# Optimization experiments

Measured on AMD Instinct MI355X. Metric: run time of the kernel, lower is better.

The kernel has to match this reference:

```python
import jax, jax.numpy as jnp
import numpy as np

B, N, D_IN, D_OUT = 4096, 200, 64, 64


def setup_inputs() -> dict:
    key = jax.random.key(0)
    k1, k2 = jax.random.split(key)
    x = jax.random.normal(k1, (B, N, D_IN), dtype=jnp.float32)
    # weight initialized like TF add_weight default (glorot-ish scale via normal here)
    weight = jax.random.normal(k2, (1, N, D_IN, D_OUT), dtype=jnp.float32) * (1.0 / np.sqrt(D_IN))
    bias = jnp.zeros((1, N, D_OUT), dtype=jnp.float32)
    return {"x": x, "weight": weight, "bias": bias}


def reference(x, weight, bias):
    # Original: (x[..., None] * weight).sum(-2) + bias
    # == per-token matmul: out[b,n,o] = sum_i x[b,n,i] * weight[0,n,i,o] + bias[0,n,o]
    out = jnp.einsum('bni,nio->bno', x, weight[0])
    return out + bias
```

## Files before the change

kernel.cpp:

```cpp
#include <hip/hip_runtime.h>


#define B_DIM 4096
#define N_DIM 200
#define D 64
#define ROWS_PER_BLOCK 256

typedef __attribute__((ext_vector_type(8))) _Float16 half8;
typedef __attribute__((ext_vector_type(4))) float f32x4;

__device__ __forceinline__ void split8(const float4 a, const float4 b,
                                       half8& h, half8& l) {
  const float f[8] = {a.x, a.y, a.z, a.w, b.x, b.y, b.z, b.w};
#pragma unroll
  for (int j = 0; j < 8; ++j) {
    const _Float16 hh = (_Float16)f[j];
    h[j] = hh;
    l[j] = (_Float16)(f[j] - (float)hh);
  }
}

__global__ __launch_bounds__(256)
void w_prep(const float* __restrict__ w,
            half8* __restrict__ wh, half8* __restrict__ wl) {
  const int n    = blockIdx.x;
  const int tid  = threadIdx.x;
  const int lane = tid & 63;
  const int g    = tid >> 6;
  const int c    = lane & 15;
  const int kg   = lane >> 4;
  const float* wn = w + (size_t)n * (D * D);
#pragma unroll
  for (int t = 0; t < 2; ++t) {
    const int combo = g * 2 + t;
    const int ks = combo >> 2;
    const int nf = combo & 3;
    half8 h, l;
#pragma unroll
    for (int j = 0; j < 8; ++j) {
      const int k = ks * 32 + kg * 8 + j;
      const float v = wn[k * D + nf * 16 + c];
      const _Float16 hh = (_Float16)v;
      h[j] = hh;
      l[j] = (_Float16)(v - (float)hh);
    }
    const size_t idx = ((size_t)(n * 2 + ks) * 4 + nf) * 64 + lane;
    wh[idx] = h;
    wl[idx] = l;
  }
}

template <bool PREPPED>
__global__ __launch_bounds__(256, 4)
void nlinear_main(const float* __restrict__ x,
                  const float* __restrict__ w,
                  const float* __restrict__ bias,
                  const half8* __restrict__ wh,
                  const half8* __restrict__ wl,
                  float* __restrict__ out) {
  const int n    = blockIdx.y;
  const int tid  = threadIdx.x;
  const int lane = tid & 63;
  const int wave = tid >> 6;
  const int c    = lane & 15;
  const int kg   = lane >> 4;

  half8 Wh[2][4], Wl[2][4];
  if (PREPPED) {
#pragma unroll
    for (int ks = 0; ks < 2; ++ks)
#pragma unroll
      for (int nf = 0; nf < 4; ++nf) {
        const size_t idx = ((size_t)(n * 2 + ks) * 4 + nf) * 64 + lane;
        Wh[ks][nf] = wh[idx];
        Wl[ks][nf] = wl[idx];
      }
  } else {
    const float* wn = w + (size_t)n * (D * D);
#pragma unroll
    for (int ks = 0; ks < 2; ++ks)
#pragma unroll
      for (int nf = 0; nf < 4; ++nf)
#pragma unroll
        for (int j = 0; j < 8; ++j) {
          const float v = wn[(ks * 32 + kg * 8 + j) * D + nf * 16 + c];
          const _Float16 hh = (_Float16)v;
          Wh[ks][nf][j] = hh;
          Wl[ks][nf][j] = (_Float16)(v - (float)hh);
        }
  }

  const float bv[4] = {bias[n * D + c],      bias[n * D + 16 + c],
                       bias[n * D + 32 + c], bias[n * D + 48 + c]};

  const size_t rstride = (size_t)N_DIM * D;
  const int row0 = blockIdx.x * ROWS_PER_BLOCK + wave * 64;
  const float* xb = x + (size_t)row0 * rstride + (size_t)n * D;
  float* ob = out + (size_t)row0 * rstride + (size_t)n * D;

  const float* xr0 = xb + (size_t)c * rstride + kg * 8;
  float4 A0 = *(const float4*)(xr0);
  float4 A1 = *(const float4*)(xr0 + 4);
  float4 A2 = *(const float4*)(xr0 + 32);
  float4 A3 = *(const float4*)(xr0 + 36);

#pragma unroll 1
  for (int mf = 0; mf < 4; ++mf) {
    const float4 v0 = A0, v1 = A1, v2 = A2, v3 = A3;
    if (mf < 3) {
      const float* xn = xb + (size_t)((mf + 1) * 16 + c) * rstride + kg * 8;
      A0 = *(const float4*)(xn);
      A1 = *(const float4*)(xn + 4);
      A2 = *(const float4*)(xn + 32);
      A3 = *(const float4*)(xn + 36);
    }

    half8 ah[2], al[2];
    split8(v0, v1, ah[0], al[0]);
    split8(v2, v3, ah[1], al[1]);

    f32x4 acc[4];
#pragma unroll
    for (int nf = 0; nf < 4; ++nf) {
      f32x4 t = {bv[nf], bv[nf], bv[nf], bv[nf]};
      acc[nf] = t;
    }

#pragma unroll
    for (int ks = 0; ks < 2; ++ks)
#pragma unroll
      for (int nf = 0; nf < 4; ++nf) {
        acc[nf] = __builtin_amdgcn_mfma_f32_16x16x32_f16(ah[ks], Wh[ks][nf], acc[nf], 0, 0, 0);
        acc[nf] = __builtin_amdgcn_mfma_f32_16x16x32_f16(ah[ks], Wl[ks][nf], acc[nf], 0, 0, 0);
        acc[nf] = __builtin_amdgcn_mfma_f32_16x16x32_f16(al[ks], Wh[ks][nf], acc[nf], 0, 0, 0);
      }

    float* orow = ob + (size_t)(mf * 16 + kg * 4) * rstride;
#pragma unroll
    for (int nf = 0; nf < 4; ++nf)
#pragma unroll
      for (int j = 0; j < 4; ++j)
        orow[(size_t)j * rstride + nf * 16 + c] = acc[nf][j];
  }
}

extern "C" void kernel_launch(void* const* d_in, const int* in_sizes, int n_in,
                              void* d_out, int out_size, void* d_ws, size_t ws_size,
                              hipStream_t stream) {
  const float* x    = (const float*)d_in[0];
  const float* w    = (const float*)d_in[1];
  const float* bias = (const float*)d_in[2];
  float*       out  = (float*)d_out;

  const size_t NFRAGS = (size_t)N_DIM * 2 * 4 * 64;
  const size_t NEED   = NFRAGS * 16 * 2;

  dim3 grid(B_DIM / ROWS_PER_BLOCK, N_DIM);
  if (d_ws && ws_size >= NEED) {
    half8* wh = (half8*)d_ws;
    half8* wl = wh + NFRAGS;
    w_prep<<<dim3(N_DIM), dim3(256), 0, stream>>>(w, wh, wl);
    nlinear_main<true><<<grid, dim3(256), 0, stream>>>(x, w, bias, wh, wl, out);
  } else {
    nlinear_main<false><<<grid, dim3(256), 0, stream>>>(x, w, bias, nullptr, nullptr, out);
  }
}
```

Before: 395.5 us.

## Transpose MFMA operands for vectorized float4 output stores and double-buffer x loads

Swaps the MFMA A/B operands so each lane's accumulator holds four consecutive output columns for one row. The epilogue can then write float4 stores instead of scalar strided stores, and bias is loaded as a float4. It also replaces the single-stage x prefetch with a two-deep register prefetch and fully unrolls the row loop. Occupancy is relaxed to 3 waves-per-EU in launch bounds to give room for the extra registers.

```diff
diff --git a/kernel.cpp b/kernel.cpp
--- a/kernel.cpp
+++ b/kernel.cpp
@@ -34,24 +34,24 @@
   for (int t = 0; t < 2; ++t) {
     const int combo = g * 2 + t;
     const int ks = combo >> 2;
-    const int nf = combo & 3;
+    const int of = combo & 3;
     half8 h, l;
 #pragma unroll
     for (int j = 0; j < 8; ++j) {
       const int k = ks * 32 + kg * 8 + j;
-      const float v = wn[k * D + nf * 16 + c];
+      const float v = wn[k * D + of * 16 + c];
       const _Float16 hh = (_Float16)v;
       h[j] = hh;
       l[j] = (_Float16)(v - (float)hh);
     }
-    const size_t idx = ((size_t)(n * 2 + ks) * 4 + nf) * 64 + lane;
+    const size_t idx = ((size_t)(n * 2 + ks) * 4 + of) * 64 + lane;
     wh[idx] = h;
     wl[idx] = l;
   }
 }
 
 template <bool PREPPED>
-__global__ __launch_bounds__(256, 4)
+__global__ __launch_bounds__(256, 3)
 void nlinear_main(const float* __restrict__ x,
                   const float* __restrict__ w,
                   const float* __restrict__ bias,
@@ -70,77 +70,92 @@
 #pragma unroll
     for (int ks = 0; ks < 2; ++ks)
 #pragma unroll
-      for (int nf = 0; nf < 4; ++nf) {
-        const size_t idx = ((size_t)(n * 2 + ks) * 4 + nf) * 64 + lane;
-        Wh[ks][nf] = wh[idx];
-        Wl[ks][nf] = wl[idx];
+      for (int of = 0; of < 4; ++of) {
+        const size_t idx = ((size_t)(n * 2 + ks) * 4 + of) * 64 + lane;
+        Wh[ks][of] = wh[idx];
+        Wl[ks][of] = wl[idx];
       }
   } else {
     const float* wn = w + (size_t)n * (D * D);
 #pragma unroll
     for (int ks = 0; ks < 2; ++ks)
 #pragma unroll
-      for (int nf = 0; nf < 4; ++nf)
+      for (int of = 0; of < 4; ++of)
 #pragma unroll
         for (int j = 0; j < 8; ++j) {
-          const float v = wn[(ks * 32 + kg * 8 + j) * D + nf * 16 + c];
+          const float v = wn[(ks * 32 + kg * 8 + j) * D + of * 16 + c];
           const _Float16 hh = (_Float16)v;
-          Wh[ks][nf][j] = hh;
-          Wl[ks][nf][j] = (_Float16)(v - (float)hh);
+          Wh[ks][of][j] = hh;
+          Wl[ks][of][j] = (_Float16)(v - (float)hh);
         }
   }
 
-  const float bv[4] = {bias[n * D + c],      bias[n * D + 16 + c],
-                       bias[n * D + 32 + c], bias[n * D + 48 + c]};
+  float4 bv4[4];
+#pragma unroll
+  for (int of = 0; of < 4; ++of)
+    bv4[of] = *(const float4*)(bias + (size_t)n * D + of * 16 + kg * 4);
 
   const size_t rstride = (size_t)N_DIM * D;
   const int row0 = blockIdx.x * ROWS_PER_BLOCK + wave * 64;
   const float* xb = x + (size_t)row0 * rstride + (size_t)n * D;
   float* ob = out + (size_t)row0 * rstride + (size_t)n * D;
 
-  const float* xr0 = xb + (size_t)c * rstride + kg * 8;
-  float4 A0 = *(const float4*)(xr0);
-  float4 A1 = *(const float4*)(xr0 + 4);
-  float4 A2 = *(const float4*)(xr0 + 32);
-  float4 A3 = *(const float4*)(xr0 + 36);
+  auto xaddr = [&](int mf) {
+    return xb + (size_t)(mf * 16 + c) * rstride + kg * 8;
+  };
 
-#pragma unroll 1
+  float4 P[2][4];
+  {
+    const float* p0 = xaddr(0);
+    P[0][0] = *(const float4*)(p0);
+    P[0][1] = *(const float4*)(p0 + 4);
+    P[0][2] = *(const float4*)(p0 + 32);
+    P[0][3] = *(const float4*)(p0 + 36);
+    const float* p1 = xaddr(1);
+    P[1][0] = *(const float4*)(p1);
+    P[1][1] = *(const float4*)(p1 + 4);
+    P[1][2] = *(const float4*)(p1 + 32);
+    P[1][3] = *(const float4*)(p1 + 36);
+  }
+
+#pragma unroll
   for (int mf = 0; mf < 4; ++mf) {
-    const float4 v0 = A0, v1 = A1, v2 = A2, v3 = A3;
-    if (mf < 3) {
-      const float* xn = xb + (size_t)((mf + 1) * 16 + c) * rstride + kg * 8;
-      A0 = *(const float4*)(xn);
-      A1 = *(const float4*)(xn + 4);
-      A2 = *(const float4*)(xn + 32);
-      A3 = *(const float4*)(xn + 36);
+    const int buf = mf & 1;
+    const float4 v0 = P[buf][0], v1 = P[buf][1];
+    const float4 v2 = P[buf][2], v3 = P[buf][3];
+    if (mf < 2) {
+      const float* pn = xaddr(mf + 2);
+      P[buf][0] = *(const float4*)(pn);
+      P[buf][1] = *(const float4*)(pn + 4);
+      P[buf][2] = *(const float4*)(pn + 32);
+      P[buf][3] = *(const float4*)(pn + 36);
     }
 
-    half8 ah[2], al[2];
-    split8(v0, v1, ah[0], al[0]);
-    split8(v2, v3, ah[1], al[1]);
+    half8 ah0, al0, ah1, al1;
+    split8(v0, v1, ah0, al0);
+    split8(v2, v3, ah1, al1);
 
     f32x4 acc[4];
 #pragma unroll
-    for (int nf = 0; nf < 4; ++nf) {
-      f32x4 t = {bv[nf], bv[nf], bv[nf], bv[nf]};
-      acc[nf] = t;
+    for (int of = 0; of < 4; ++of) {
+      f32x4 t = {bv4[of].x, bv4[of].y, bv4[of].z, bv4[of].w};
+      acc[of] = t;
     }
 
 #pragma unroll
-    for (int ks = 0; ks < 2; ++ks)
+    for (int of = 0; of < 4; ++of) {
+      acc[of] = __builtin_amdgcn_mfma_f32_16x16x32_f16(Wh[0][of], ah0, acc[of], 0, 0, 0);
+      acc[of] = __builtin_amdgcn_mfma_f32_16x16x32_f16(Wl[0][of], ah0, acc[of], 0, 0, 0);
+      acc[of] = __builtin_amdgcn_mfma_f32_16x16x32_f16(Wh[0][of], al0, acc[of], 0, 0, 0);
+      acc[of] = __builtin_amdgcn_mfma_f32_16x16x32_f16(Wh[1][of], ah1, acc[of], 0, 0, 0);
+      acc[of] = __builtin_amdgcn_mfma_f32_16x16x32_f16(Wl[1][of], ah1, acc[of], 0, 0, 0);
+      acc[of] = __builtin_amdgcn_mfma_f32_16x16x32_f16(Wh[1][of], al1, acc[of], 0, 0, 0);
+    }
+
+    float* orow = ob + (size_t)(mf * 16 + c) * rstride;
 #pragma unroll
-      for (int nf = 0; nf < 4; ++nf) {
-        acc[nf] = __builtin_amdgcn_mfma_f32_16x16x32_f16(ah[ks], Wh[ks][nf], acc[nf], 0, 0, 0);
-        acc[nf] = __builtin_amdgcn_mfma_f32_16x16x32_f16(ah[ks], Wl[ks][nf], acc[nf], 0, 0, 0);
-        acc[nf] = __builtin_amdgcn_mfma_f32_16x16x32_f16(al[ks], Wh[ks][nf], acc[nf], 0, 0, 0);
-      }
-
-    float* orow = ob + (size_t)(mf * 16 + kg * 4) * rstride;
-#pragma unroll
-    for (int nf = 0; nf < 4; ++nf)
-#pragma unroll
-      for (int j = 0; j < 4; ++j)
-        orow[(size_t)j * rstride + nf * 16 + c] = acc[nf][j];
+    for (int of = 0; of < 4; ++of)
+      *(f32x4*)(orow + of * 16 + kg * 4) = acc[of];
   }
 }
 
@@ -157,10 +172,10 @@
 
   dim3 grid(B_DIM / ROWS_PER_BLOCK, N_DIM);
   if (d_ws && ws_size >= NEED) {
-    half8* wh = (half8*)d_ws;
-    half8* wl = wh + NFRAGS;
-    w_prep<<<dim3(N_DIM), dim3(256), 0, stream>>>(w, wh, wl);
-    nlinear_main<true><<<grid, dim3(256), 0, stream>>>(x, w, bias, wh, wl, out);
+    half8* whp = (half8*)d_ws;
+    half8* wlp = whp + NFRAGS;
+    w_prep<<<dim3(N_DIM), dim3(256), 0, stream>>>(w, whp, wlp);
+    nlinear_main<true><<<grid, dim3(256), 0, stream>>>(x, w, bias, whp, wlp, out);
   } else {
     nlinear_main<false><<<grid, dim3(256), 0, stream>>>(x, w, bias, nullptr, nullptr, out);
   }
```

Result: faster. 377.3 us (-4.6%).
